# Kernel optimization log

Measured on AMD Instinct MI355X. Metric: run time of the kernel, lower is better.

Reference implementation:

```python
import jax, jax.numpy as jnp
import numpy as np

N = 50000       # nodes
E = 600000      # directed edges (before self loops)
IN_CH = 128
HID = 64
HEADS = 2
H2_CH = HID // HEADS  # 32
OUT_CH = 96
NEG_SLOPE = 0.2


def _w(key, shape):
    fan_in = shape[-1]
    return jax.random.normal(key, shape, dtype=jnp.float32) / np.sqrt(fan_in).astype(np.float32)


def setup_inputs() -> dict:
    key = jax.random.key(0)
    ks = jax.random.split(key, 20)
    x = jax.random.normal(ks[0], (N, IN_CH), dtype=jnp.float32)
    edge_index = jax.random.randint(ks[1], (2, E), 0, N, dtype=jnp.int32)
    batch = jnp.zeros((N,), dtype=jnp.int32)
    return {
        "x": x, "edge_index": edge_index, "batch": batch,
        # lin_in 128->128
        "Win": _w(ks[2], (IN_CH, IN_CH)), "b_in": jnp.zeros((IN_CH,), jnp.float32),
        # conv1: GATv2Conv(128 -> 64, heads=2, concat=True)
        "Wl1": _w(ks[3], (HEADS * HID, IN_CH)), "bl1": jnp.zeros((HEADS * HID,), jnp.float32),
        "Wr1": _w(ks[4], (HEADS * HID, IN_CH)), "br1": jnp.zeros((HEADS * HID,), jnp.float32),
        "att1": _w(ks[5], (HEADS, HID)), "bias1": jnp.zeros((HEADS * HID,), jnp.float32),
        # conv2: GATv2Conv(128 -> 32, heads=1, concat=True)
        "Wl2": _w(ks[6], (H2_CH, HEADS * HID)), "bl2": jnp.zeros((H2_CH,), jnp.float32),
        "Wr2": _w(ks[7], (H2_CH, HEADS * HID)), "br2": jnp.zeros((H2_CH,), jnp.float32),
        "att2": _w(ks[8], (1, H2_CH)), "bias2": jnp.zeros((H2_CH,), jnp.float32),
        # final linear 32 -> 96
        "Wout": _w(ks[9], (OUT_CH, H2_CH)), "b_out": jnp.zeros((OUT_CH,), jnp.float32),
    }


def _segment_softmax(logits, seg, num):
    # logits: [E, H] grouped by seg (destination node); every node has a self loop.
    m = jax.ops.segment_max(logits, seg, num_segments=num)
    ex = jnp.exp(logits - m[seg])
    s = jax.ops.segment_sum(ex, seg, num_segments=num)
    return ex / s[seg]


def _gatv2_conv(h, Wl, bl, Wr, br, att, bias, src, dst, heads, ch):
    n = h.shape[0]
    xl = (h @ Wl.T + bl).reshape(n, heads, ch)  # source-side (x_j)
    xr = (h @ Wr.T + br).reshape(n, heads, ch)  # target-side (x_i)
    e = jax.nn.leaky_relu(xl[src] + xr[dst], NEG_SLOPE)       # [E, H, C]
    logits = jnp.einsum('ehc,hc->eh', e, att)                  # [E, H]
    alpha = _segment_softmax(logits, dst, n)                   # softmax over in-edges per dst
    out = jax.ops.segment_sum(alpha[:, :, None] * xl[src], dst, num_segments=n)
    return out.reshape(n, heads * ch) + bias


def reference(x, edge_index, batch, Win, b_in, Wl1, bl1, Wr1, br1, att1, bias1,
              Wl2, bl2, Wr2, br2, att2, bias2, Wout, b_out):
    n = x.shape[0]
    loops = jnp.arange(n, dtype=edge_index.dtype)
    src = jnp.concatenate([edge_index[0], loops])  # add_self_loops=True (PyG default)
    dst = jnp.concatenate([edge_index[1], loops])
    h = x @ Win.T + b_in
    h = jax.nn.relu(_gatv2_conv(h, Wl1, bl1, Wr1, br1, att1, bias1, src, dst, HEADS, HID))
    h = jax.nn.relu(_gatv2_conv(h, Wl2, bl2, Wr2, br2, att2, bias2, src, dst, 1, H2_CH))
    num_graphs = 1
    sums = jax.ops.segment_sum(h, batch, num_segments=num_graphs)          # [G, 32]
    cnt = jax.ops.segment_sum(jnp.ones((n,), h.dtype), batch, num_segments=num_graphs)
    pooled = sums / cnt[:, None]
    return pooled @ Wout.T + b_out  # [G, 96]
```

## Files before the change

### kernel.cpp

```cpp
#include <hip/hip_runtime.h>
#include <hip/hip_bf16.h>
#include <math.h>


#define NEG_SLOPE 0.2f
#define LOG2E 1.4426950408889634f
#define NREP 16
#define ELLW 64

typedef __attribute__((ext_vector_type(8))) short bf16x8;
typedef __attribute__((ext_vector_type(4))) float f32x4;

__device__ __forceinline__ float leaky(float t) { return fmaxf(t, NEG_SLOPE * t); }
__device__ __forceinline__ float bf2f(unsigned short u) {
    return __uint_as_float((unsigned)u << 16);
}
__device__ __forceinline__ short f2bf(float f) {
    __hip_bfloat16 h = __float2bfloat16(f);
    return *reinterpret_cast<short*>(&h);
}
__device__ __forceinline__ short f2bf_fast(float f) {
    return (short)((__float_as_uint(f) + 0x8000u) >> 16);
}

__global__ __launch_bounds__(256) void prep_kernel(const float* __restrict__ Win,
                                                   const float* __restrict__ b_in,
                                                   const float* __restrict__ Wl1,
                                                   const float* __restrict__ bl1,
                                                   const float* __restrict__ Wr1,
                                                   const float* __restrict__ br1,
                                                   const float* __restrict__ Wl2,
                                                   const float* __restrict__ bl2,
                                                   const float* __restrict__ Wr2,
                                                   const float* __restrict__ br2,
                                                   unsigned short* __restrict__ Wcat1,
                                                   float* __restrict__ bcat1,
                                                   unsigned short* __restrict__ Wcat2,
                                                   float* __restrict__ bcat2,
                                                   int* __restrict__ cursor,
                                                   float* __restrict__ pooledR, int N) {
    int b = blockIdx.x, t = threadIdx.x;
    if (b < 128) {
        int half = t >> 7;
        int k = t & 127;
        int o = b * 2 + half;
        const float* Wx = (o < 128) ? Wl1 : Wr1;
        const float* bx = (o < 128) ? bl1 : br1;
        int oo = o & 127;
        float acc = 0.f;
#pragma unroll 16
        for (int j = 0; j < 128; ++j)
            acc = fmaf(Wx[oo * 128 + j], Win[j * 128 + k], acc);
        Wcat1[o * 128 + k] = (unsigned short)f2bf(acc);

        __shared__ float red[256];
        red[t] = Wx[oo * 128 + k] * b_in[k];
        __syncthreads();
        for (int off = 64; off > 0; off >>= 1) {
            if (k < off) red[t] += red[t + off];
            __syncthreads();
        }
        if (k == 0) bcat1[o] = red[half * 128] + bx[oo];
    } else if (b < 160) {
        int i = (b - 128) * 256 + t;
        int m = i >> 7, kk = i & 127;
        float v = (m < 32) ? Wl2[m * 128 + kk] : Wr2[(m - 32) * 128 + kk];
        Wcat2[i] = (unsigned short)f2bf(v);
        if (b == 128 && t < 64) bcat2[t] = (t < 32) ? bl2[t] : br2[t - 32];
    } else {
        int zb = b - 160;
        for (int i = zb * 256 + t; i < N; i += 96 * 256) cursor[i] = 0;
        for (int i = zb * 256 + t; i < NREP * 32; i += 96 * 256) pooledR[i] = 0.f;
    }
}

__global__ __launch_bounds__(256) void gemm1s_kernel(const float* __restrict__ x,
                                                     const unsigned short* __restrict__ W,
                                                     const float* __restrict__ bias,
                                                     unsigned short* __restrict__ XL,
                                                     unsigned short* __restrict__ XR,
                                                     int N,
                                                     const int* __restrict__ ei,
                                                     int* __restrict__ cursor,
                                                     unsigned short* __restrict__ ell,
                                                     int E) {
    const int w = threadIdx.x >> 6;
    const int lane = threadIdx.x & 63;
    const int ln = lane & 15;
    const int quad = lane >> 4;
    const int nb = blockIdx.x * 32;
    const int c0 = w * 64;

    int rows[2];
#pragma unroll
    for (int rt = 0; rt < 2; ++rt) {
        int n = nb + rt * 16 + ln;
        rows[rt] = n < N ? n : N - 1;
    }

    float4 araw[2][4][2];
#pragma unroll
    for (int rt = 0; rt < 2; ++rt)
#pragma unroll
        for (int kc = 0; kc < 4; ++kc) {
            const float* p = x + (size_t)rows[rt] * 128 + kc * 32 + quad * 8;
            araw[rt][kc][0] = *(const float4*)p;
            araw[rt][kc][1] = *(const float4*)(p + 4);
        }
    bf16x8 a[2][4];
#pragma unroll
    for (int rt = 0; rt < 2; ++rt)
#pragma unroll
        for (int kc = 0; kc < 4; ++kc) {
            float4 u = araw[rt][kc][0], v = araw[rt][kc][1];
            a[rt][kc][0] = f2bf_fast(u.x); a[rt][kc][1] = f2bf_fast(u.y);
            a[rt][kc][2] = f2bf_fast(u.z); a[rt][kc][3] = f2bf_fast(u.w);
            a[rt][kc][4] = f2bf_fast(v.x); a[rt][kc][5] = f2bf_fast(v.y);
            a[rt][kc][6] = f2bf_fast(v.z); a[rt][kc][7] = f2bf_fast(v.w);
        }

    f32x4 acc[2][4];
#pragma unroll
    for (int rt = 0; rt < 2; ++rt)
#pragma unroll
        for (int ct = 0; ct < 4; ++ct) acc[rt][ct] = (f32x4){0.f, 0.f, 0.f, 0.f};

#pragma unroll
    for (int kc = 0; kc < 4; ++kc) {
        const int k0 = kc * 32 + quad * 8;
        bf16x8 wv[4];
#pragma unroll
        for (int ct = 0; ct < 4; ++ct)
            wv[ct] = *(const bf16x8*)(W + (size_t)(c0 + ct * 16 + ln) * 128 + k0);
#pragma unroll
        for (int rt = 0; rt < 2; ++rt)
#pragma unroll
            for (int ct = 0; ct < 4; ++ct)
                acc[rt][ct] = __builtin_amdgcn_mfma_f32_16x16x32_bf16(wv[ct], a[rt][kc], acc[rt][ct], 0, 0, 0);
    }

#pragma unroll
    for (int rt = 0; rt < 2; ++rt) {
        int n = nb + rt * 16 + ln;
        if (n < N) {
#pragma unroll
            for (int ct = 0; ct < 4; ++ct) {
                int cb = c0 + ct * 16 + quad * 4;
                float4 bv = *(const float4*)&bias[cb];
                ushort4 o;
                o.x = (unsigned short)f2bf(acc[rt][ct][0] + bv.x);
                o.y = (unsigned short)f2bf(acc[rt][ct][1] + bv.y);
                o.z = (unsigned short)f2bf(acc[rt][ct][2] + bv.z);
                o.w = (unsigned short)f2bf(acc[rt][ct][3] + bv.w);
                if (cb < 128) *(ushort4*)&XL[(size_t)n * 128 + cb] = o;
                else          *(ushort4*)&XR[(size_t)n * 128 + cb - 128] = o;
            }
        }
    }

    for (int e = blockIdx.x * 256 + threadIdx.x; e < E; e += gridDim.x * 256) {
        int s = ei[e];
        int d = ei[E + e];
        int r = atomicAdd(&cursor[d], 1);
        if (r < ELLW) ell[(size_t)d * ELLW + r] = (unsigned short)s;
    }
}

__global__ __launch_bounds__(256) void gemm2_kernel(const unsigned short* __restrict__ A,
                                                    const unsigned short* __restrict__ W,
                                                    const float* __restrict__ bias,
                                                    unsigned short* __restrict__ OUT0,
                                                    unsigned short* __restrict__ OUT1,
                                                    int N) {
    const int w = threadIdx.x >> 6;
    const int lane = threadIdx.x & 63;
    const int ln = lane & 15;
    const int quad = lane >> 4;
    const int nb = blockIdx.x * 64;
    const int c0 = w * 16;

    f32x4 acc[4];
#pragma unroll
    for (int rt = 0; rt < 4; ++rt) acc[rt] = (f32x4){0.f, 0.f, 0.f, 0.f};

    int rows[4];
#pragma unroll
    for (int rt = 0; rt < 4; ++rt) {
        int n = nb + rt * 16 + ln;
        rows[rt] = n < N ? n : N - 1;
    }

#pragma unroll
    for (int kc = 0; kc < 4; ++kc) {
        const int k0 = kc * 32 + quad * 8;
        bf16x8 a[4];
#pragma unroll
        for (int rt = 0; rt < 4; ++rt)
            a[rt] = *(const bf16x8*)(A + (size_t)rows[rt] * 128 + k0);
        bf16x8 wv = *(const bf16x8*)(W + (size_t)(c0 + ln) * 128 + k0);
#pragma unroll
        for (int rt = 0; rt < 4; ++rt)
            acc[rt] = __builtin_amdgcn_mfma_f32_16x16x32_bf16(wv, a[rt], acc[rt], 0, 0, 0);
    }

#pragma unroll
    for (int rt = 0; rt < 4; ++rt) {
        int n = nb + rt * 16 + ln;
        if (n >= N) continue;
        int cb = c0 + quad * 4;
        float4 bv = *(const float4*)&bias[cb];
        ushort4 o;
        o.x = (unsigned short)f2bf(acc[rt][0] + bv.x);
        o.y = (unsigned short)f2bf(acc[rt][1] + bv.y);
        o.z = (unsigned short)f2bf(acc[rt][2] + bv.z);
        o.w = (unsigned short)f2bf(acc[rt][3] + bv.w);
        if (cb < 32) *(ushort4*)&OUT0[(size_t)n * 32 + cb] = o;
        else         *(ushort4*)&OUT1[(size_t)n * 32 + cb - 32] = o;
    }
}

__global__ __launch_bounds__(256) void node_conv1(const unsigned short* __restrict__ XL,
                                                  const unsigned short* __restrict__ XR,
                                                  const int* __restrict__ deg,
                                                  const unsigned short* __restrict__ ell,
                                                  const float* __restrict__ att,
                                                  const float* __restrict__ bias,
                                                  unsigned short* __restrict__ H1, int N) {
    int d = blockIdx.x * 8 + (threadIdx.x >> 5);
    if (d >= N) return;
    int l = threadIdx.x & 31;
    int c0 = 4 * l;
    const unsigned short* row = ell + (size_t)d * ELLW;
    int re = deg[d];
    if (re > ELLW) re = ELLW;

    float4 attv = *(const float4*)&att[c0];
    attv.x *= LOG2E; attv.y *= LOG2E; attv.z *= LOG2E; attv.w *= LOG2E;
    ushort4 xru = *(const ushort4*)&XR[(size_t)d * 128 + c0];
    float xr0 = bf2f(xru.x), xr1 = bf2f(xru.y), xr2 = bf2f(xru.z), xr3 = bf2f(xru.w);

    float ssum = 0.f, a0 = 0.f, a1 = 0.f, a2 = 0.f, a3 = 0.f;

#define LOADX1(j) (*(const ushort4*)&XL[(size_t)row[(j) < re ? (j) : re - 1] * 128 + c0])
#define PROC1(xu)                                                          \
    {                                                                      \
        float x0 = bf2f(xu.x), x1 = bf2f(xu.y), x2 = bf2f(xu.z), x3 = bf2f(xu.w); \
        float p = leaky(x0 + xr0) * attv.x;                                \
        p = fmaf(leaky(x1 + xr1), attv.y, p);                              \
        p = fmaf(leaky(x2 + xr2), attv.z, p);                              \
        p = fmaf(leaky(x3 + xr3), attv.w, p);                              \
        p += __shfl_xor(p, 8, 16);                                         \
        p += __shfl_xor(p, 4, 16);                                         \
        p += __shfl_xor(p, 2, 16);                                         \
        p += __shfl_xor(p, 1, 16);                                         \
        float wgt = exp2f(p);                                              \
        ssum += wgt;                                                       \
        a0 = fmaf(wgt, x0, a0); a1 = fmaf(wgt, x1, a1);                    \
        a2 = fmaf(wgt, x2, a2); a3 = fmaf(wgt, x3, a3);                    \
    }

    {
        ushort4 xls = *(const ushort4*)&XL[(size_t)d * 128 + c0];
        PROC1(xls);
    }
    if (re > 0) {
        ushort4 b0 = LOADX1(0), b1 = LOADX1(1), b2 = LOADX1(2), b3 = LOADX1(3);
        for (int j = 0; j < re; j += 4) {
            ushort4 n0 = LOADX1(j + 4), n1 = LOADX1(j + 5), n2 = LOADX1(j + 6), n3 = LOADX1(j + 7);
            PROC1(b0);
            if (j + 1 < re) PROC1(b1);
            if (j + 2 < re) PROC1(b2);
            if (j + 3 < re) PROC1(b3);
            b0 = n0; b1 = n1; b2 = n2; b3 = n3;
        }
    }
#undef PROC1
#undef LOADX1

    float inv = 1.0f / ssum;
    float4 bv = *(const float4*)&bias[c0];
    float r0 = fmaf(a0, inv, bv.x), r1 = fmaf(a1, inv, bv.y);
    float r2 = fmaf(a2, inv, bv.z), r3 = fmaf(a3, inv, bv.w);
    ushort4 o;
    o.x = (unsigned short)f2bf(r0 > 0.f ? r0 : 0.f);
    o.y = (unsigned short)f2bf(r1 > 0.f ? r1 : 0.f);
    o.z = (unsigned short)f2bf(r2 > 0.f ? r2 : 0.f);
    o.w = (unsigned short)f2bf(r3 > 0.f ? r3 : 0.f);
    *(ushort4*)&H1[(size_t)d * 128 + c0] = o;
}

__global__ __launch_bounds__(256) void node_conv2(const unsigned short* __restrict__ XL,
                                                  const unsigned short* __restrict__ XR,
                                                  const int* __restrict__ deg,
                                                  const unsigned short* __restrict__ ell,
                                                  const float* __restrict__ att,
                                                  const float* __restrict__ bias,
                                                  float* __restrict__ pooledR, int N) {
    __shared__ float psh[32];
    if (threadIdx.x < 32) psh[threadIdx.x] = 0.0f;
    __syncthreads();

    int slot = threadIdx.x >> 3;
    int l = threadIdx.x & 7;
    int c0 = 4 * l;
    float4 attv = *(const float4*)&att[c0];
    attv.x *= LOG2E; attv.y *= LOG2E; attv.z *= LOG2E; attv.w *= LOG2E;
    float4 bv = *(const float4*)&bias[c0];
    float p0 = 0.f, p1 = 0.f, p2 = 0.f, p3 = 0.f;

#define LOADX2(j) (*(const ushort4*)&XL[(size_t)row[(j) < re ? (j) : re - 1] * 32 + c0])
#define PROC2(xu)                                                          \
    {                                                                      \
        float x0 = bf2f(xu.x), x1 = bf2f(xu.y), x2 = bf2f(xu.z), x3 = bf2f(xu.w); \
        float p = leaky(x0 + xr0) * attv.x;                                \
        p = fmaf(leaky(x1 + xr1), attv.y, p);                              \
        p = fmaf(leaky(x2 + xr2), attv.z, p);                              \
        p = fmaf(leaky(x3 + xr3), attv.w, p);                              \
        p += __shfl_xor(p, 4, 8);                                          \
        p += __shfl_xor(p, 2, 8);                                          \
        p += __shfl_xor(p, 1, 8);                                          \
        float wgt = exp2f(p);                                              \
        ssum += wgt;                                                       \
        a0 = fmaf(wgt, x0, a0); a1 = fmaf(wgt, x1, a1);                    \
        a2 = fmaf(wgt, x2, a2); a3 = fmaf(wgt, x3, a3);                    \
    }

    for (int d = blockIdx.x * 32 + slot; d < N; d += gridDim.x * 32) {
        const unsigned short* row = ell + (size_t)d * ELLW;
        int re = deg[d];
        if (re > ELLW) re = ELLW;
        ushort4 xru = *(const ushort4*)&XR[(size_t)d * 32 + c0];
        float xr0 = bf2f(xru.x), xr1 = bf2f(xru.y), xr2 = bf2f(xru.z), xr3 = bf2f(xru.w);
        float ssum = 0.f, a0 = 0.f, a1 = 0.f, a2 = 0.f, a3 = 0.f;

        {
            ushort4 xls = *(const ushort4*)&XL[(size_t)d * 32 + c0];
            PROC2(xls);
        }
        if (re > 0) {
            ushort4 b0 = LOADX2(0), b1 = LOADX2(1), b2 = LOADX2(2), b3 = LOADX2(3);
            for (int j = 0; j < re; j += 4) {
                ushort4 n0 = LOADX2(j + 4), n1 = LOADX2(j + 5), n2 = LOADX2(j + 6), n3 = LOADX2(j + 7);
                PROC2(b0);
                if (j + 1 < re) PROC2(b1);
                if (j + 2 < re) PROC2(b2);
                if (j + 3 < re) PROC2(b3);
                b0 = n0; b1 = n1; b2 = n2; b3 = n3;
            }
        }

        float inv = 1.0f / ssum;
        float r0 = fmaf(a0, inv, bv.x), r1 = fmaf(a1, inv, bv.y);
        float r2 = fmaf(a2, inv, bv.z), r3 = fmaf(a3, inv, bv.w);
        p0 += r0 > 0.f ? r0 : 0.f;
        p1 += r1 > 0.f ? r1 : 0.f;
        p2 += r2 > 0.f ? r2 : 0.f;
        p3 += r3 > 0.f ? r3 : 0.f;
    }
#undef PROC2
#undef LOADX2
    atomicAdd(&psh[c0 + 0], p0);
    atomicAdd(&psh[c0 + 1], p1);
    atomicAdd(&psh[c0 + 2], p2);
    atomicAdd(&psh[c0 + 3], p3);
    __syncthreads();
    float* rep = pooledR + (blockIdx.x & (NREP - 1)) * 32;
    if (threadIdx.x < 32) atomicAdd(&rep[threadIdx.x], psh[threadIdx.x]);
}

__global__ void out_kernel(const float* __restrict__ pooledR, const float* __restrict__ Wout,
                           const float* __restrict__ b_out, float* __restrict__ out, int N) {
    __shared__ float psum[32];
    if (threadIdx.x < 32) {
        float tot = 0.f;
#pragma unroll
        for (int r = 0; r < NREP; ++r) tot += pooledR[r * 32 + threadIdx.x];
        psum[threadIdx.x] = tot;
    }
    __syncthreads();
    int m = threadIdx.x;
    if (m < 96) {
        float invN = 1.0f / (float)N;
        float s = b_out[m];
#pragma unroll
        for (int c = 0; c < 32; ++c) s += (psum[c] * invN) * Wout[m * 32 + c];
        out[m] = s;
    }
}

extern "C" void kernel_launch(void* const* d_in, const int* in_sizes, int n_in,
                              void* d_out, int out_size, void* d_ws, size_t ws_size,
                              hipStream_t stream) {
    const float* x     = (const float*)d_in[0];
    const int*   ei    = (const int*)d_in[1];
    const float* Win   = (const float*)d_in[3];
    const float* b_in  = (const float*)d_in[4];
    const float* Wl1   = (const float*)d_in[5];
    const float* bl1   = (const float*)d_in[6];
    const float* Wr1   = (const float*)d_in[7];
    const float* br1   = (const float*)d_in[8];
    const float* att1  = (const float*)d_in[9];
    const float* bias1 = (const float*)d_in[10];
    const float* Wl2   = (const float*)d_in[11];
    const float* bl2   = (const float*)d_in[12];
    const float* Wr2   = (const float*)d_in[13];
    const float* br2   = (const float*)d_in[14];
    const float* att2  = (const float*)d_in[15];
    const float* bias2 = (const float*)d_in[16];
    const float* Wout  = (const float*)d_in[17];
    const float* b_out = (const float*)d_in[18];
    float* out = (float*)d_out;

    int N = in_sizes[0] / 128;
    int E = in_sizes[1] / 2;

    char* wsb = (char*)d_ws;
    size_t off = 0;
    auto alloc = [&](size_t bytes) { void* p = wsb + off; off += (bytes + 255) & ~(size_t)255; return p; };

    unsigned short* XL1   = (unsigned short*)alloc((size_t)N * 128 * 2);
    unsigned short* XR1   = (unsigned short*)alloc((size_t)N * 128 * 2);
    unsigned short* H1    = (unsigned short*)alloc((size_t)N * 128 * 2);
    unsigned short* Wcat1 = (unsigned short*)alloc(256 * 128 * 2);
    unsigned short* Wcat2 = (unsigned short*)alloc(64 * 128 * 2);
    float* bcat1   = (float*)alloc(256 * 4);
    float* bcat2   = (float*)alloc(64 * 4);
    float* pooledR = (float*)alloc(NREP * 32 * 4);
    int* cursor    = (int*)alloc((size_t)N * 4);
    unsigned short* ell = (unsigned short*)alloc((size_t)N * ELLW * 2);
    unsigned short* XL2 = XL1;
    unsigned short* XR2 = XR1;

    prep_kernel<<<256, 256, 0, stream>>>(Win, b_in, Wl1, bl1, Wr1, br1,
                                         Wl2, bl2, Wr2, br2,
                                         Wcat1, bcat1, Wcat2, bcat2, cursor, pooledR, N);
    gemm1s_kernel<<<(N + 31) / 32, 256, 0, stream>>>(x, Wcat1, bcat1, XL1, XR1, N,
                                                     ei, cursor, ell, E);
    node_conv1<<<(N + 7) / 8, 256, 0, stream>>>(XL1, XR1, cursor, ell, att1, bias1, H1, N);
    gemm2_kernel<<<(N + 63) / 64, 256, 0, stream>>>(H1, Wcat2, bcat2, XL2, XR2, N);
    node_conv2<<<1024, 256, 0, stream>>>(XL2, XR2, cursor, ell, att2, bias2, pooledR, N);
    out_kernel<<<1, 128, 0, stream>>>(pooledR, Wout, b_out, out, N);
}
```

Before: 231.9 us.

## Build ELL adjacency via two-pass bucket partition with shared-memory assembly

Replaces the per-edge global atomic scatter into the ELL table (previously fused into the first GEMM) with a two-pass scheme. Edges are first partitioned into 256-node buckets using block-local histograms, then each bucket's ELL rows are assembled in shared memory and written out coalesced. This removes random global atomics and scattered 2-byte stores and produces a clamped degree array. The cost is two extra kernel launches and a staging buffer with a fixed per-bucket capacity that could overflow on skewed graphs. The 256-entry bucket counter and 16-bit packing assume fewer than 65536 nodes.

```diff
diff --git a/kernel.cpp b/kernel.cpp
--- a/kernel.cpp
+++ b/kernel.cpp
@@ -7,6 +7,8 @@
 #define LOG2E 1.4426950408889634f
 #define NREP 16
 #define ELLW 64
+#define CH 2048
+#define CAPB 8192
 
 typedef __attribute__((ext_vector_type(8))) short bf16x8;
 typedef __attribute__((ext_vector_type(4))) float f32x4;
@@ -37,7 +39,7 @@
                                                    float* __restrict__ bcat1,
                                                    unsigned short* __restrict__ Wcat2,
                                                    float* __restrict__ bcat2,
-                                                   int* __restrict__ cursor,
+                                                   int* __restrict__ bucketCnt,
                                                    float* __restrict__ pooledR, int N) {
     int b = blockIdx.x, t = threadIdx.x;
     if (b < 128) {
@@ -67,23 +69,85 @@
         float v = (m < 32) ? Wl2[m * 128 + kk] : Wr2[(m - 32) * 128 + kk];
         Wcat2[i] = (unsigned short)f2bf(v);
         if (b == 128 && t < 64) bcat2[t] = (t < 32) ? bl2[t] : br2[t - 32];
+    } else if (b == 160) {
+        if (t < 256) bucketCnt[t] = 0;
     } else {
-        int zb = b - 160;
-        for (int i = zb * 256 + t; i < N; i += 96 * 256) cursor[i] = 0;
-        for (int i = zb * 256 + t; i < NREP * 32; i += 96 * 256) pooledR[i] = 0.f;
-    }
-}
-
-__global__ __launch_bounds__(256) void gemm1s_kernel(const float* __restrict__ x,
-                                                     const unsigned short* __restrict__ W,
-                                                     const float* __restrict__ bias,
-                                                     unsigned short* __restrict__ XL,
-                                                     unsigned short* __restrict__ XR,
-                                                     int N,
-                                                     const int* __restrict__ ei,
-                                                     int* __restrict__ cursor,
-                                                     unsigned short* __restrict__ ell,
-                                                     int E) {
+        int i = (b - 161) * 256 + t;
+        if (i < NREP * 32) pooledR[i] = 0.f;
+    }
+}
+
+__global__ __launch_bounds__(256) void part_kernel(const int* __restrict__ ei,
+                                                   int* __restrict__ bucketCnt,
+                                                   unsigned int* __restrict__ region,
+                                                   int E) {
+    __shared__ int hist[256];
+    __shared__ int base[256];
+    __shared__ int off[256];
+    int b = blockIdx.x, t = threadIdx.x;
+    int e0 = b * CH;
+    int e1 = e0 + CH; if (e1 > E) e1 = E;
+
+    hist[t] = 0;
+    __syncthreads();
+    for (int e = e0 + t; e < e1; e += 256) {
+        int d = ei[E + e];
+        atomicAdd(&hist[d >> 8], 1);
+    }
+    __syncthreads();
+    int h = hist[t];
+    base[t] = (h > 0) ? atomicAdd(&bucketCnt[t], h) : 0;
+    off[t] = 0;
+    __syncthreads();
+    for (int e = e0 + t; e < e1; e += 256) {
+        int s = ei[e];
+        int d = ei[E + e];
+        int bk = d >> 8;
+        int p = base[bk] + atomicAdd(&off[bk], 1);
+        if (p < CAPB)
+            region[(size_t)bk * CAPB + p] = (unsigned)s | ((unsigned)(d & 255) << 16);
+    }
+}
+
+__global__ __launch_bounds__(256) void ellb_kernel(const unsigned int* __restrict__ region,
+                                                   const int* __restrict__ bucketCnt,
+                                                   unsigned short* __restrict__ ell,
+                                                   int* __restrict__ deg, int N) {
+    __shared__ unsigned short tile[256 * ELLW];
+    __shared__ int cur[256];
+    int nb = blockIdx.x, t = threadIdx.x;
+    cur[t] = 0;
+    __syncthreads();
+    int cnt = bucketCnt[nb];
+    if (cnt > CAPB) cnt = CAPB;
+    for (int i = t; i < cnt; i += 256) {
+        unsigned p = region[(size_t)nb * CAPB + i];
+        int doff = p >> 16;
+        int s = p & 0xFFFF;
+        int r = atomicAdd(&cur[doff], 1);
+        if (r < ELLW) tile[doff * ELLW + r] = (unsigned short)s;
+    }
+    __syncthreads();
+    int node = nb * 256 + t;
+    if (node < N) {
+        int dgl = cur[t];
+        deg[node] = dgl < ELLW ? dgl : ELLW;
+    }
+    const uint4* tl = (const uint4*)tile;
+    uint4* gl = (uint4*)(ell + (size_t)nb * 256 * ELLW);
+#pragma unroll
+    for (int k = 0; k < 8; ++k) {
+        int idx = t + k * 256;
+        int row = idx >> 3;
+        if (nb * 256 + row < N) gl[idx] = tl[idx];
+    }
+}
+
+__global__ __launch_bounds__(256) void gemm1_kernel(const float* __restrict__ x,
+                                                    const unsigned short* __restrict__ W,
+                                                    const float* __restrict__ bias,
+                                                    unsigned short* __restrict__ XL,
+                                                    unsigned short* __restrict__ XR, int N) {
     const int w = threadIdx.x >> 6;
     const int lane = threadIdx.x & 63;
     const int ln = lane & 15;
@@ -142,27 +206,19 @@
 #pragma unroll
     for (int rt = 0; rt < 2; ++rt) {
         int n = nb + rt * 16 + ln;
-        if (n < N) {
-#pragma unroll
-            for (int ct = 0; ct < 4; ++ct) {
-                int cb = c0 + ct * 16 + quad * 4;
-                float4 bv = *(const float4*)&bias[cb];
-                ushort4 o;
-                o.x = (unsigned short)f2bf(acc[rt][ct][0] + bv.x);
-                o.y = (unsigned short)f2bf(acc[rt][ct][1] + bv.y);
-                o.z = (unsigned short)f2bf(acc[rt][ct][2] + bv.z);
-                o.w = (unsigned short)f2bf(acc[rt][ct][3] + bv.w);
-                if (cb < 128) *(ushort4*)&XL[(size_t)n * 128 + cb] = o;
-                else          *(ushort4*)&XR[(size_t)n * 128 + cb - 128] = o;
-            }
-        }
-    }
-
-    for (int e = blockIdx.x * 256 + threadIdx.x; e < E; e += gridDim.x * 256) {
-        int s = ei[e];
-        int d = ei[E + e];
-        int r = atomicAdd(&cursor[d], 1);
-        if (r < ELLW) ell[(size_t)d * ELLW + r] = (unsigned short)s;
+        if (n >= N) continue;
+#pragma unroll
+        for (int ct = 0; ct < 4; ++ct) {
+            int cb = c0 + ct * 16 + quad * 4;
+            float4 bv = *(const float4*)&bias[cb];
+            ushort4 o;
+            o.x = (unsigned short)f2bf(acc[rt][ct][0] + bv.x);
+            o.y = (unsigned short)f2bf(acc[rt][ct][1] + bv.y);
+            o.z = (unsigned short)f2bf(acc[rt][ct][2] + bv.z);
+            o.w = (unsigned short)f2bf(acc[rt][ct][3] + bv.w);
+            if (cb < 128) *(ushort4*)&XL[(size_t)n * 128 + cb] = o;
+            else          *(ushort4*)&XR[(size_t)n * 128 + cb - 128] = o;
+        }
     }
 }
 
@@ -232,7 +288,6 @@
     int c0 = 4 * l;
     const unsigned short* row = ell + (size_t)d * ELLW;
     int re = deg[d];
-    if (re > ELLW) re = ELLW;
 
     float4 attv = *(const float4*)&att[c0];
     attv.x *= LOG2E; attv.y *= LOG2E; attv.z *= LOG2E; attv.w *= LOG2E;
@@ -241,7 +296,7 @@
 
     float ssum = 0.f, a0 = 0.f, a1 = 0.f, a2 = 0.f, a3 = 0.f;
 
-#define LOADX1(j) (*(const ushort4*)&XL[(size_t)row[(j) < re ? (j) : re - 1] * 128 + c0])
+#define LOADX1(j) (*(const ushort4*)&XL[(size_t)row[(j) < re ? (j) : (re > 0 ? re - 1 : 0)] * 128 + c0])
 #define PROC1(xu)                                                          \
     {                                                                      \
         float x0 = bf2f(xu.x), x1 = bf2f(xu.y), x2 = bf2f(xu.z), x3 = bf2f(xu.w); \
@@ -308,7 +363,7 @@
     float4 bv = *(const float4*)&bias[c0];
     float p0 = 0.f, p1 = 0.f, p2 = 0.f, p3 = 0.f;
 
-#define LOADX2(j) (*(const ushort4*)&XL[(size_t)row[(j) < re ? (j) : re - 1] * 32 + c0])
+#define LOADX2(j) (*(const ushort4*)&XL[(size_t)row[(j) < re ? (j) : (re > 0 ? re - 1 : 0)] * 32 + c0])
 #define PROC2(xu)                                                          \
     {                                                                      \
         float x0 = bf2f(xu.x), x1 = bf2f(xu.y), x2 = bf2f(xu.z), x3 = bf2f(xu.w); \
@@ -328,7 +383,6 @@
     for (int d = blockIdx.x * 32 + slot; d < N; d += gridDim.x * 32) {
         const unsigned short* row = ell + (size_t)d * ELLW;
         int re = deg[d];
-        if (re > ELLW) re = ELLW;
         ushort4 xru = *(const ushort4*)&XR[(size_t)d * 32 + c0];
         float xr0 = bf2f(xru.x), xr1 = bf2f(xru.y), xr2 = bf2f(xru.z), xr3 = bf2f(xru.w);
         float ssum = 0.f, a0 = 0.f, a1 = 0.f, a2 = 0.f, a3 = 0.f;
@@ -413,6 +467,7 @@
 
     int N = in_sizes[0] / 128;
     int E = in_sizes[1] / 2;
+    int NB = (N + 255) >> 8;
 
     char* wsb = (char*)d_ws;
     size_t off = 0;
@@ -426,18 +481,21 @@
     float* bcat1   = (float*)alloc(256 * 4);
     float* bcat2   = (float*)alloc(64 * 4);
     float* pooledR = (float*)alloc(NREP * 32 * 4);
-    int* cursor    = (int*)alloc((size_t)N * 4);
-    unsigned short* ell = (unsigned short*)alloc((size_t)N * ELLW * 2);
+    int* bucketCnt = (int*)alloc(256 * 4);
+    int* deg       = (int*)alloc((size_t)N * 4);
+    unsigned int* region = (unsigned int*)alloc((size_t)NB * CAPB * 4);
+    unsigned short* ell  = (unsigned short*)alloc((size_t)N * ELLW * 2);
     unsigned short* XL2 = XL1;
     unsigned short* XR2 = XR1;
 
-    prep_kernel<<<256, 256, 0, stream>>>(Win, b_in, Wl1, bl1, Wr1, br1,
+    prep_kernel<<<163, 256, 0, stream>>>(Win, b_in, Wl1, bl1, Wr1, br1,
                                          Wl2, bl2, Wr2, br2,
-                                         Wcat1, bcat1, Wcat2, bcat2, cursor, pooledR, N);
-    gemm1s_kernel<<<(N + 31) / 32, 256, 0, stream>>>(x, Wcat1, bcat1, XL1, XR1, N,
-                                                     ei, cursor, ell, E);
-    node_conv1<<<(N + 7) / 8, 256, 0, stream>>>(XL1, XR1, cursor, ell, att1, bias1, H1, N);
+                                         Wcat1, bcat1, Wcat2, bcat2, bucketCnt, pooledR, N);
+    part_kernel<<<(E + CH - 1) / CH, 256, 0, stream>>>(ei, bucketCnt, region, E);
+    ellb_kernel<<<NB, 256, 0, stream>>>(region, bucketCnt, ell, deg, N);
+    gemm1_kernel<<<(N + 31) / 32, 256, 0, stream>>>(x, Wcat1, bcat1, XL1, XR1, N);
+    node_conv1<<<(N + 7) / 8, 256, 0, stream>>>(XL1, XR1, deg, ell, att1, bias1, H1, N);
     gemm2_kernel<<<(N + 63) / 64, 256, 0, stream>>>(H1, Wcat2, bcat2, XL2, XR2, N);
-    node_conv2<<<1024, 256, 0, stream>>>(XL2, XR2, cursor, ell, att2, bias2, pooledR, N);
+    node_conv2<<<1024, 256, 0, stream>>>(XL2, XR2, deg, ell, att2, bias2, pooledR, N);
     out_kernel<<<1, 128, 0, stream>>>(pooledR, Wout, b_out, out, N);
 }
```

Result: no change. 229.5 us (-1.1%).
